# Performance work log

Measured on AMD Instinct MI355X. Metric: run time of the kernel, lower is better.

The kernel has to match this reference:

```python
import jax, jax.numpy as jnp
import numpy as np

N = 6000
E = 192000
H = 128
NUM_HEADS = 4

def _segsum(x, idx, n):
    return jax.ops.segment_sum(x, idx, num_segments=n)

def _gcn_encode(x, edges, W0, b0, Ws, bs):
    n = x.shape[0]
    sl = jnp.arange(n, dtype=edges.dtype)
    row = jnp.concatenate([edges[0], sl])  # source
    col = jnp.concatenate([edges[1], sl])  # target (aggregation)
    deg = _segsum(jnp.ones_like(col, dtype=x.dtype), col, n)
    dinv = jax.lax.rsqrt(deg)  # deg >= 1 thanks to self loops
    norm = (dinv[row] * dinv[col])[:, None]
    def layer(h, W, b):
        hw = h @ W
        agg = _segsum(hw[row] * norm, col, n)
        return jax.nn.relu(agg + b)
    h = layer(x, W0, b0)
    for i in range(Ws.shape[0]):
        h = layer(h, Ws[i], bs[i])
    return h

def setup_inputs() -> dict:
    key = jax.random.key(0)
    ks = jax.random.split(key, 24)
    def lin(k, fan_in, shape):
        return jax.random.normal(k, shape, dtype=jnp.float32) / np.sqrt(fan_in)
    return {
        'x_resting': jax.random.normal(ks[0], (N, 3), dtype=jnp.float32),
        'x_rigid': jax.random.normal(ks[1], (N, 3), dtype=jnp.float32),
        'edge_resting': jax.random.randint(ks[2], (2, E), 0, N, dtype=jnp.int32),
        'edge_rigid': jax.random.randint(ks[3], (2, E), 0, N, dtype=jnp.int32),
        'Wr0': lin(ks[4], 3, (3, H)), 'br0': jnp.zeros((H,), jnp.float32),
        'Wr': lin(ks[5], H, (2, H, H)), 'br': jnp.zeros((2, H), jnp.float32),
        'Wg0': lin(ks[6], 3, (3, H)), 'bg0': jnp.zeros((H,), jnp.float32),
        'Wg': lin(ks[7], H, (2, H, H)), 'bg': jnp.zeros((2, H), jnp.float32),
        'Wa': lin(ks[8], H, (NUM_HEADS, H, H)), 'ba': jnp.zeros((NUM_HEADS, H), jnp.float32),
        'Wd0': lin(ks[9], H * (NUM_HEADS + 1), (H * (NUM_HEADS + 1), H)), 'bd0': jnp.zeros((H,), jnp.float32),
        'Wd': lin(ks[10], H, (2, H, H)), 'bd': jnp.zeros((2, H), jnp.float32),
        'Wout': lin(ks[11], H, (H, 3)), 'bout': jnp.zeros((3,), jnp.float32),
    }

def reference(x_resting, x_rigid, edge_resting, edge_rigid,
              Wr0, br0, Wr, br, Wg0, bg0, Wg, bg,
              Wa, ba, Wd0, bd0, Wd, bd, Wout, bout):
    xr = _gcn_encode(x_resting, edge_resting, Wr0, br0, Wr, br)  # (N,H)
    xg = _gcn_encode(x_rigid, edge_rigid, Wg0, bg0, Wg, bg)      # (N,H)

    def head(W, b):
        q = xr @ W + b            # (N,H)
        k = xg @ W + b            # (N,H)
        attn = jax.nn.softmax(q @ k.T, axis=-1)  # (N,N) dense per head
        return attn @ xg          # (N,H)
    heads = jax.vmap(head)(Wa, ba)                       # (heads,N,H)
    pooled = heads.transpose(1, 0, 2).reshape(xr.shape[0], -1)  # (N, heads*H)

    h = jnp.concatenate([xr, pooled], axis=-1)  # (N, H*(heads+1))
    h = jax.nn.relu(h @ Wd0 + bd0)
    for i in range(Wd.shape[0]):
        h = jax.nn.relu(h @ Wd[i] + bd[i])
    return h @ Wout + bout  # (N, 3) deformed positions
```

## Files before the change

### kernel.cpp

```cpp
#include <hip/hip_runtime.h>
#include <math.h>

#define N_NODES 6000
#define N_EDGES 192000
#define H 128
#define NHEADS 4
#define HCAT 640
#define NPAD 6016
#define NTILES 188

typedef unsigned short ushort_t;
typedef __attribute__((ext_vector_type(8))) short short8;
typedef __attribute__((ext_vector_type(16))) float f32x16;

__device__ __forceinline__ void bf16split(float x, ushort_t& hi, ushort_t& lo) {
    unsigned ub = __float_as_uint(x);
    unsigned hb = ub & 0xffff0000u;
    float l = x - __uint_as_float(hb);
    hi = (ushort_t)(hb >> 16);
    lo = (ushort_t)(__float_as_uint(l) >> 16);
}

__device__ __forceinline__ void gll16(const ushort_t* g, ushort_t* l) {
    __builtin_amdgcn_global_load_lds((const __attribute__((address_space(1))) void*)g,
                                     (__attribute__((address_space(3))) void*)l, 16, 0, 0);
}

__global__ void zero_ints(int* p, int n) {
    int i = blockIdx.x * 256 + threadIdx.x;
    if (i < n) p[i] = 0;
}

__global__ void hist2(const int* __restrict__ eA, const int* __restrict__ eB,
                      int* __restrict__ cnt) {
    int e = blockIdx.x * 256 + threadIdx.x;
    int z = blockIdx.y;
    const int* edges = z ? eB : eA;
    if (e < N_EDGES) atomicAdd(&cnt[z * N_NODES + edges[N_EDGES + e]], 1);
}

__global__ __launch_bounds__(1024)
void scan2(const int* __restrict__ cnt_all, int* __restrict__ rs_all,
           float* __restrict__ dinv_all) {
    __shared__ int ps[1024];
    int z = blockIdx.x;
    const int* cnt = cnt_all + z * N_NODES;
    int* row_start = rs_all + z * (N_NODES + 1);
    float* dinv = dinv_all + z * N_NODES;
    int t = threadIdx.x;
    int base = t * 6;
    int local[6];
    int s = 0;
#pragma unroll
    for (int j = 0; j < 6; ++j) {
        int idx = base + j;
        int v = (idx < N_NODES) ? cnt[idx] : 0;
        local[j] = s;
        s += v;
        if (idx < N_NODES) dinv[idx] = rsqrtf((float)(v + 1));
    }
    ps[t] = s;
    __syncthreads();
    for (int off = 1; off < 1024; off <<= 1) {
        int v = (t >= off) ? ps[t - off] : 0;
        __syncthreads();
        ps[t] += v;
        __syncthreads();
    }
    int ex = (t > 0) ? ps[t - 1] : 0;
#pragma unroll
    for (int j = 0; j < 6; ++j) {
        int idx = base + j;
        if (idx < N_NODES) row_start[idx] = ex + local[j];
    }
    if (t == 1023) row_start[N_NODES] = ps[1023];
}

__global__ void place2(const int* __restrict__ eA, const int* __restrict__ eB,
                       const int* __restrict__ rs_all, int* __restrict__ cur_all,
                       int* __restrict__ eslot_all) {
    int e = blockIdx.x * 256 + threadIdx.x;
    int z = blockIdx.y;
    const int* edges = z ? eB : eA;
    if (e < N_EDGES) {
        int tg = edges[N_EDGES + e];
        int p = atomicAdd(&cur_all[z * N_NODES + tg], 1);
        eslot_all[(size_t)z * N_EDGES + rs_all[z * (N_NODES + 1) + tg] + p] = e;
    }
}

__global__ __launch_bounds__(256)
void gather_x3(const float* __restrict__ xA, const float* __restrict__ xB,
               const int* __restrict__ eA, const int* __restrict__ eB,
               const int* __restrict__ eslot_all, const int* __restrict__ rs_all,
               const float* __restrict__ dinv_all,
               float* __restrict__ outA, float* __restrict__ outB) {
    int z = blockIdx.y;
    int n = blockIdx.x * 256 + threadIdx.x;
    if (n >= N_NODES) return;
    const int* edges = z ? eB : eA;
    const int* eslot = eslot_all + (size_t)z * N_EDGES;
    const int* row_start = rs_all + z * (N_NODES + 1);
    const float* x = z ? xB : xA;
    const float* dv = dinv_all + z * N_NODES;
    float* out = z ? outB : outA;
    float di = dv[n];
    float a0 = x[n * 3 + 0] * di * di;
    float a1 = x[n * 3 + 1] * di * di;
    float a2 = x[n * 3 + 2] * di * di;
    int s0 = row_start[n], s1 = row_start[n + 1];
    for (int i = s0; i < s1; ++i) {
        int e = eslot[i];
        int s = edges[e];
        float nr = dv[s] * di;
        a0 += x[s * 3 + 0] * nr;
        a1 += x[s * 3 + 1] * nr;
        a2 += x[s * 3 + 2] * nr;
    }
    out[n * 3 + 0] = a0; out[n * 3 + 1] = a1; out[n * 3 + 2] = a2;
}

__global__ __launch_bounds__(256)
void gcn_gemm2(const float* __restrict__ hinA, const float* __restrict__ hinB,
               const float* __restrict__ WA, const float* __restrict__ WB,
               float* __restrict__ hwA, float* __restrict__ hwB, int in_dim,
               const float* __restrict__ bA, const float* __restrict__ bB, int do_relu) {
    __shared__ float xs[16 * H];
    int z = blockIdx.y;
    const float* hin = z ? hinB : hinA;
    const float* W = z ? WB : WA;
    float* hw = z ? hwB : hwA;
    const float* b = z ? bB : bA;
    int n0 = blockIdx.x * 16;
    int t = threadIdx.x;
    int f = t & (H - 1);
    int g = t >> 7;
    for (int i = t; i < 16 * H; i += 256) {
        int r = i >> 7, c = i & (H - 1);
        xs[i] = (c < in_dim) ? hin[(size_t)(n0 + r) * in_dim + c] : 0.f;
    }
    __syncthreads();
    float acc[8];
#pragma unroll
    for (int j = 0; j < 8; ++j) acc[j] = 0.f;
    for (int d = 0; d < in_dim; ++d) {
        float w = W[d * H + f];
#pragma unroll
        for (int j = 0; j < 8; ++j) acc[j] += xs[(g * 8 + j) * H + d] * w;
    }
    if (do_relu) {
        float bias = b[f];
#pragma unroll
        for (int j = 0; j < 8; ++j)
            hw[(size_t)(n0 + g * 8 + j) * H + f] = fmaxf(acc[j] + bias, 0.f);
    } else {
#pragma unroll
        for (int j = 0; j < 8; ++j) hw[(size_t)(n0 + g * 8 + j) * H + f] = acc[j];
    }
}

__global__ __launch_bounds__(H)
void gather2(const int* __restrict__ eA, const int* __restrict__ eB,
             const int* __restrict__ eslot_all, const int* __restrict__ rs_all,
             const float* __restrict__ hwA, const float* __restrict__ hwB,
             const float* __restrict__ dinv_all,
             const float* __restrict__ bA, const float* __restrict__ bB,
             float* __restrict__ outA, float* __restrict__ outB, int osA, int osB) {
    __shared__ int ssrc[128];
    __shared__ float snrm[128];
    int z = blockIdx.y;
    const int* edges = z ? eB : eA;
    const int* eslot = eslot_all + (size_t)z * N_EDGES;
    const int* row_start = rs_all + z * (N_NODES + 1);
    const float* hw = z ? hwB : hwA;
    const float* dinv = dinv_all + z * N_NODES;
    const float* b = z ? bB : bA;
    float* out = z ? outB : outA;
    int ostride = z ? osB : osA;

    int tg = blockIdx.x, f = threadIdx.x;
    int s0 = row_start[tg], s1 = row_start[tg + 1];
    float di = dinv[tg];
    float acc = hw[(size_t)tg * H + f] * di * di;
    for (int base = s0; base < s1; base += 128) {
        int cnt = min(128, s1 - base);
        __syncthreads();
        if (f < cnt) {
            int e = eslot[base + f];
            int s = edges[e];
            ssrc[f] = s;
            snrm[f] = dinv[s] * di;
        }
        __syncthreads();
        for (int i = 0; i < cnt; ++i)
            acc += hw[(size_t)ssrc[i] * H + f] * snrm[i];
    }
    float v = acc + b[f];
    out[(size_t)tg * ostride + f] = v > 0.f ? v : 0.f;
}

__global__ __launch_bounds__(256)
void qk_kernel2(const float* __restrict__ qs, int qstride, const float* __restrict__ xg,
                const float* __restrict__ Wa, const float* __restrict__ ba,
                ushort_t* __restrict__ Qh, ushort_t* __restrict__ Ql,
                ushort_t* __restrict__ Khs, ushort_t* __restrict__ Kls) {
    __shared__ float xs[2][16][H];
    int n0 = blockIdx.x * 16, head = blockIdx.y;
    int t = threadIdx.x;
    int f = t & (H - 1);
    int g = t >> 7;
    for (int i = t; i < 2 * 16 * H; i += 256) {
        int which = i >> 11;
        int rem = i & 2047;
        int row = rem >> 7, col = rem & 127;
        xs[which][row][col] = which ? xg[(size_t)(n0 + row) * H + col]
                                    : qs[(size_t)(n0 + row) * qstride + col];
    }
    __syncthreads();
    const float* W = Wa + (size_t)head * H * H;
    float bias = ba[head * H + f];
    float acc[16];
#pragma unroll
    for (int j = 0; j < 16; ++j) acc[j] = bias;
    for (int d = 0; d < H; ++d) {
        float w = W[d * H + f];
#pragma unroll
        for (int j = 0; j < 16; ++j) acc[j] += xs[g][j][d] * w;
    }
#pragma unroll
    for (int j = 0; j < 16; ++j) {
        int n = n0 + j;
        ushort_t hi, lo;
        bf16split(acc[j], hi, lo);
        if (g == 0) {
            size_t idx = ((size_t)(head * N_NODES + n) << 7) + f;
            Qh[idx] = hi; Ql[idx] = lo;
        } else {
            int pos = (((f >> 3) ^ (n & 15)) << 3) + (f & 7);
            size_t idx = ((size_t)(head * NPAD + n) << 7) + pos;
            Khs[idx] = hi; Kls[idx] = lo;
        }
    }
}

__global__ void zero_pad_k(ushort_t* __restrict__ Khs, ushort_t* __restrict__ Kls) {
    int i = blockIdx.x * 256 + threadIdx.x;
    if (i < NHEADS * 16 * H) {
        int head = i / (16 * H);
        int rest = i - head * 16 * H;
        int n = N_NODES + (rest >> 7);
        int f = rest & 127;
        size_t idx = ((size_t)(head * NPAD + n) << 7) + f;
        Khs[idx] = 0; Kls[idx] = 0;
    }
}

__global__ __launch_bounds__(128)
void cvt_vt(const float* __restrict__ xg, ushort_t* __restrict__ Vth, ushort_t* __restrict__ Vtl) {
    __shared__ float vs[32][129];
    int t0 = blockIdx.x;
    int t = threadIdx.x;
    for (int c = t; c < 32 * 32; c += 128) {
        int row = c >> 5, col4 = (c & 31) << 2;
        int n = t0 * 32 + row;
        float4 v = (n < N_NODES) ? *(const float4*)&xg[(size_t)n * H + col4]
                                 : float4{0.f, 0.f, 0.f, 0.f};
        vs[row][col4 + 0] = v.x; vs[row][col4 + 1] = v.y;
        vs[row][col4 + 2] = v.z; vs[row][col4 + 3] = v.w;
    }
    __syncthreads();
    int d = t;
    size_t base = ((size_t)t0 * H + d) * 32;
#pragma unroll
    for (int oc = 0; oc < 4; ++oc) {
        int cc = oc ^ (d & 3);
        unsigned uh[4], ul[4];
#pragma unroll
        for (int j = 0; j < 4; ++j) {
            ushort_t h0, l0, h1, l1;
            bf16split(vs[cc * 8 + 2 * j][d], h0, l0);
            bf16split(vs[cc * 8 + 2 * j + 1][d], h1, l1);
            uh[j] = (unsigned)h0 | ((unsigned)h1 << 16);
            ul[j] = (unsigned)l0 | ((unsigned)l1 << 16);
        }
        *(uint4*)&Vth[base + oc * 8] = make_uint4(uh[0], uh[1], uh[2], uh[3]);
        *(uint4*)&Vtl[base + oc * 8] = make_uint4(ul[0], ul[1], ul[2], ul[3]);
    }
}

__global__ __launch_bounds__(256, 2)
void attn_mfma7(const ushort_t* __restrict__ Qh, const ushort_t* __restrict__ Ql,
                const ushort_t* __restrict__ Khs, const ushort_t* __restrict__ Kls,
                const ushort_t* __restrict__ Vth, const ushort_t* __restrict__ Vtl,
                float* __restrict__ Opart, float* __restrict__ mlpart, int tps) {
    __shared__ ushort_t lds[2][4][4096];
    const int head = blockIdx.y;
    const int sp = blockIdx.z;
    const int t = threadIdx.x;
    const int lane = t & 63;
    const int w = t >> 6;
    const int r = lane & 31;
    const int h = lane >> 5;
    const int q0w = blockIdx.x * 128 + w * 32;

    int t_begin = sp * tps;
    int t_end = t_begin + tps; if (t_end > NTILES) t_end = NTILES;

    const size_t kbase = (size_t)head * NPAD * H;
    const int o1 = t * 8, o2 = t * 8 + 2048;

    int qr = q0w + r; if (qr > N_NODES - 1) qr = N_NODES - 1;
    const size_t qbase = ((size_t)(head * N_NODES + qr)) << 7;
    short8 qfh[8], qfl[8];
#pragma unroll
    for (int s = 0; s < 8; ++s) {
        qfh[s] = *(const short8*)&Qh[qbase + 16 * s + 8 * h];
        qfl[s] = *(const short8*)&Ql[qbase + 16 * s + 8 * h];
    }

    f32x16 O[4];
#pragma unroll
    for (int sub = 0; sub < 4; ++sub)
#pragma unroll
        for (int i = 0; i < 16; ++i) O[sub][i] = 0.f;
    float mrun = -1e30f, lrun = 0.f;
    short8 aPh[2], aPl[2];
    float alpha_prev = 1.f;
    int resc_prev = 0;

    {
        const ushort_t* sKh = Khs + kbase + (size_t)t_begin * 4096;
        const ushort_t* sKl = Kls + kbase + (size_t)t_begin * 4096;
        gll16(sKh + o1, &lds[0][0][o1]); gll16(sKh + o2, &lds[0][0][o2]);
        gll16(sKl + o1, &lds[0][1][o1]); gll16(sKl + o2, &lds[0][1][o2]);
    }

    for (int it = t_begin; it < t_end; ++it) {
        const int b = (it - t_begin) & 1;
        __syncthreads();
        {
            int nt = it + 1; if (nt >= t_end) nt = t_begin;
            const ushort_t* sKh = Khs + kbase + (size_t)nt * 4096;
            const ushort_t* sKl = Kls + kbase + (size_t)nt * 4096;
            const ushort_t* sVh = Vth + (size_t)it * 4096;
            const ushort_t* sVl = Vtl + (size_t)it * 4096;
            gll16(sKh + o1, &lds[b ^ 1][0][o1]); gll16(sKh + o2, &lds[b ^ 1][0][o2]);
            gll16(sKl + o1, &lds[b ^ 1][1][o1]); gll16(sKl + o2, &lds[b ^ 1][1][o2]);
            gll16(sVh + o1, &lds[b ^ 1][2][o1]); gll16(sVh + o2, &lds[b ^ 1][2][o2]);
            gll16(sVl + o1, &lds[b ^ 1][3][o1]); gll16(sVl + o2, &lds[b ^ 1][3][o2]);
        }
        const ushort_t* lKh = &lds[b][0][0];
        const ushort_t* lKl = &lds[b][1][0];
        const ushort_t* lVh = &lds[b][2][0];
        const ushort_t* lVl = &lds[b][3][0];

        f32x16 acc;
#pragma unroll
        for (int i = 0; i < 16; ++i) acc[i] = 0.f;
        const int krow = r * H;
#pragma unroll
        for (int s = 0; s < 8; ++s) {
            int cc = ((2 * s + h) ^ (r & 15)) << 3;
            short8 ah = *(const short8*)&lKh[krow + cc];
            short8 al = *(const short8*)&lKl[krow + cc];
            acc = __builtin_amdgcn_mfma_f32_32x32x16_bf16(ah, qfh[s], acc, 0, 0, 0);
            acc = __builtin_amdgcn_mfma_f32_32x32x16_bf16(ah, qfl[s], acc, 0, 0, 0);
            acc = __builtin_amdgcn_mfma_f32_32x32x16_bf16(al, qfh[s], acc, 0, 0, 0);
        }

        if (it != t_begin) {
            if (resc_prev) {
#pragma unroll
                for (int i = 0; i < 16; ++i) {
                    int rowq = (i & 3) + 8 * (i >> 2) + 4 * h;
                    float a = __shfl(alpha_prev, rowq);
#pragma unroll
                    for (int sub = 0; sub < 4; ++sub) O[sub][i] *= a;
                }
            }
#pragma unroll
            for (int sub = 0; sub < 4; ++sub) {
                const int vrow = (32 * sub + r) * 32;
#pragma unroll
                for (int s2 = 0; s2 < 2; ++s2) {
                    int cc = (((2 * s2 + h) ^ (r & 3)) << 3);
                    short8 bh = *(const short8*)&lVh[vrow + cc];
                    short8 bl = *(const short8*)&lVl[vrow + cc];
                    O[sub] = __builtin_amdgcn_mfma_f32_32x32x16_bf16(aPh[s2], bh, O[sub], 0, 0, 0);
                    O[sub] = __builtin_amdgcn_mfma_f32_32x32x16_bf16(aPh[s2], bl, O[sub], 0, 0, 0);
                    O[sub] = __builtin_amdgcn_mfma_f32_32x32x16_bf16(aPl[s2], bh, O[sub], 0, 0, 0);
                }
            }
        }

        float sv[16];
#pragma unroll
        for (int i = 0; i < 16; ++i) sv[i] = acc[i];
        int klim = N_NODES - (it << 5);
        if (klim < 32) {
#pragma unroll
            for (int i = 0; i < 16; ++i) {
                int row = (i & 3) + 8 * (i >> 2) + 4 * h;
                if (row >= klim) sv[i] = -1e30f;
            }
        }
        float tmax = sv[0];
#pragma unroll
        for (int i = 1; i < 16; ++i) tmax = fmaxf(tmax, sv[i]);
        tmax = fmaxf(tmax, __shfl_xor(tmax, 32));
        float mnew = fmaxf(mrun, tmax);
        float p[16];
        float psum = 0.f;
#pragma unroll
        for (int i = 0; i < 16; ++i) { p[i] = __expf(sv[i] - mnew); psum += p[i]; }

        if (__ballot(mnew > mrun)) {
            float alpha = __expf(mrun - mnew);
            lrun *= alpha;
            alpha_prev = alpha;
            resc_prev = 1;
        } else {
            resc_prev = 0;
        }
        lrun += psum;
        mrun = mnew;

        float pr[16];
#pragma unroll
        for (int i = 0; i < 16; ++i) pr[i] = __shfl_xor(p[i], 32);
#pragma unroll
        for (int s2 = 0; s2 < 2; ++s2) {
#pragma unroll
            for (int j = 0; j < 8; ++j) {
                int c = j & 3;
                float v;
                if (j < 4) v = (h == 0) ? p[c + 8 * s2] : pr[c + 8 * s2 + 4];
                else       v = (h == 1) ? p[c + 8 * s2 + 4] : pr[c + 8 * s2];
                unsigned ub = __float_as_uint(v);
                unsigned hb = ub & 0xffff0000u;
                float lo = v - __uint_as_float(hb);
                aPh[s2][j] = (short)(hb >> 16);
                aPl[s2][j] = (short)(__float_as_uint(lo) >> 16);
            }
        }
    }

    __syncthreads();
    {
        const int bl = (t_end - t_begin) & 1;
        const ushort_t* lVh = &lds[bl][2][0];
        const ushort_t* lVl = &lds[bl][3][0];
        if (resc_prev) {
#pragma unroll
            for (int i = 0; i < 16; ++i) {
                int rowq = (i & 3) + 8 * (i >> 2) + 4 * h;
                float a = __shfl(alpha_prev, rowq);
#pragma unroll
                for (int sub = 0; sub < 4; ++sub) O[sub][i] *= a;
            }
        }
#pragma unroll
        for (int sub = 0; sub < 4; ++sub) {
            const int vrow = (32 * sub + r) * 32;
#pragma unroll
            for (int s2 = 0; s2 < 2; ++s2) {
                int cc = (((2 * s2 + h) ^ (r & 3)) << 3);
                short8 bh = *(const short8*)&lVh[vrow + cc];
                short8 bl = *(const short8*)&lVl[vrow + cc];
                O[sub] = __builtin_amdgcn_mfma_f32_32x32x16_bf16(aPh[s2], bh, O[sub], 0, 0, 0);
                O[sub] = __builtin_amdgcn_mfma_f32_32x32x16_bf16(aPh[s2], bl, O[sub], 0, 0, 0);
                O[sub] = __builtin_amdgcn_mfma_f32_32x32x16_bf16(aPl[s2], bh, O[sub], 0, 0, 0);
            }
        }
    }

    lrun += __shfl_xor(lrun, 32);

    float* Ob = Opart + (size_t)(sp * NHEADS + head) * NPAD * H;
#pragma unroll
    for (int i = 0; i < 16; ++i) {
        int rowq = (i & 3) + 8 * (i >> 2) + 4 * h;
        int qg = q0w + rowq;
        if (qg < N_NODES) {
            float* dst = &Ob[(size_t)qg * H + r];
#pragma unroll
            for (int sub = 0; sub < 4; ++sub) dst[32 * sub] = O[sub][i];
        }
    }
    if (h == 0 && q0w + r < N_NODES) {
        float2* ml = (float2*)mlpart;
        ml[(size_t)(sp * NHEADS + head) * NPAD + q0w + r] = make_float2(mrun, lrun);
    }
}

__global__ __launch_bounds__(256)
void attn_combine(const float* __restrict__ Opart, const float* __restrict__ mlpart,
                  float* __restrict__ hcat, int ns) {
    int idx = blockIdx.x * 256 + threadIdx.x;
    if (idx >= NHEADS * N_NODES * (H / 4)) return;
    int head = idx / (N_NODES * (H / 4));
    int rest = idx - head * N_NODES * (H / 4);
    int q = rest >> 5;
    int d4 = (rest & 31) << 2;
    const float2* ml = (const float2*)mlpart;
    float m = -1e30f;
    for (int s = 0; s < ns; ++s)
        m = fmaxf(m, ml[(size_t)(s * NHEADS + head) * NPAD + q].x);
    float lsum = 0.f;
    float4 o = {0.f, 0.f, 0.f, 0.f};
    for (int s = 0; s < ns; ++s) {
        float2 v = ml[(size_t)(s * NHEADS + head) * NPAD + q];
        float wgt = __expf(v.x - m);
        lsum += v.y * wgt;
        float4 ov = *(const float4*)&Opart[((size_t)(s * NHEADS + head) * NPAD + q) * H + d4];
        o.x += ov.x * wgt; o.y += ov.y * wgt; o.z += ov.z * wgt; o.w += ov.w * wgt;
    }
    float inv = 1.f / lsum;
    float4 res = {o.x * inv, o.y * inv, o.z * inv, o.w * inv};
    *(float4*)&hcat[(size_t)q * HCAT + H + head * H + d4] = res;
}

__global__ __launch_bounds__(256)
void decoder(const float* __restrict__ hcat,
             const float* __restrict__ Wd0, const float* __restrict__ bd0,
             const float* __restrict__ Wd, const float* __restrict__ bd,
             const float* __restrict__ Wout, const float* __restrict__ bout,
             float* __restrict__ out) {
    __shared__ float s0[8 * HCAT];
    __shared__ float s1[8 * H];
    __shared__ float s2[8 * H];
    int n0 = blockIdx.x * 8;
    int t = threadIdx.x;
    int f = t & (H - 1);
    int g = t >> 7;
    for (int i = t; i < 8 * HCAT; i += 256)
        s0[i] = hcat[(size_t)n0 * HCAT + i];
    __syncthreads();

    float acc[4];
#pragma unroll
    for (int j = 0; j < 4; ++j) acc[j] = bd0[f];
    for (int d = 0; d < HCAT; ++d) {
        float w = Wd0[d * H + f];
#pragma unroll
        for (int j = 0; j < 4; ++j) acc[j] += s0[(g * 4 + j) * HCAT + d] * w;
    }
#pragma unroll
    for (int j = 0; j < 4; ++j) s1[(g * 4 + j) * H + f] = fmaxf(acc[j], 0.f);
    __syncthreads();

#pragma unroll
    for (int j = 0; j < 4; ++j) acc[j] = bd[f];
    for (int d = 0; d < H; ++d) {
        float w = Wd[d * H + f];
#pragma unroll
        for (int j = 0; j < 4; ++j) acc[j] += s1[(g * 4 + j) * H + d] * w;
    }
#pragma unroll
    for (int j = 0; j < 4; ++j) s2[(g * 4 + j) * H + f] = fmaxf(acc[j], 0.f);
    __syncthreads();

#pragma unroll
    for (int j = 0; j < 4; ++j) acc[j] = bd[H + f];
    for (int d = 0; d < H; ++d) {
        float w = Wd[H * H + d * H + f];
#pragma unroll
        for (int j = 0; j < 4; ++j) acc[j] += s2[(g * 4 + j) * H + d] * w;
    }
    __syncthreads();
#pragma unroll
    for (int j = 0; j < 4; ++j) s1[(g * 4 + j) * H + f] = fmaxf(acc[j], 0.f);
    __syncthreads();

    if (t < 24) {
        int n = t / 3, c = t % 3;
        float o = bout[c];
        for (int d = 0; d < H; ++d) o += s1[n * H + d] * Wout[d * 3 + c];
        out[(size_t)(n0 + n) * 3 + c] = o;
    }
}

extern "C" void kernel_launch(void* const* d_in, const int* in_sizes, int n_in,
                              void* d_out, int out_size, void* d_ws, size_t ws_size,
                              hipStream_t stream) {
    const float* x_rest = (const float*)d_in[0];
    const float* x_rig  = (const float*)d_in[1];
    const int*   e_rest = (const int*)d_in[2];
    const int*   e_rig  = (const int*)d_in[3];
    const float* Wr0 = (const float*)d_in[4];
    const float* br0 = (const float*)d_in[5];
    const float* Wr  = (const float*)d_in[6];
    const float* br  = (const float*)d_in[7];
    const float* Wg0 = (const float*)d_in[8];
    const float* bg0 = (const float*)d_in[9];
    const float* Wg  = (const float*)d_in[10];
    const float* bg  = (const float*)d_in[11];
    const float* Wa  = (const float*)d_in[12];
    const float* ba  = (const float*)d_in[13];
    const float* Wd0 = (const float*)d_in[14];
    const float* bd0 = (const float*)d_in[15];
    const float* Wd  = (const float*)d_in[16];
    const float* bd  = (const float*)d_in[17];
    const float* Wout = (const float*)d_in[18];
    const float* bout = (const float*)d_in[19];
    float* out = (float*)d_out;

    const size_t NH = (size_t)N_NODES * H;
    float* ws = (float*)d_ws;
    float* dinv = ws;
    float* hw   = dinv + 2 * N_NODES;
    float* hb   = hw + 2 * NH;
    float* hcat = hb + 2 * NH;
    float* ha   = hcat;
    float* xg   = hb + NH;
    float* xagg = hb;
    ushort_t* Qh  = (ushort_t*)(hcat + (size_t)N_NODES * HCAT);
    ushort_t* Ql  = Qh + (size_t)NHEADS * N_NODES * H;
    ushort_t* Khs = Ql + (size_t)NHEADS * N_NODES * H;
    ushort_t* Kls = Khs + (size_t)NHEADS * NPAD * H;
    ushort_t* Vth = Kls + (size_t)NHEADS * NPAD * H;
    ushort_t* Vtl = Vth + (size_t)NTILES * H * 32;
    int* ib   = (int*)(Vtl + (size_t)NTILES * H * 32);
    int* cnt  = ib;
    int* cur  = cnt + 2 * N_NODES;
    int* rs   = cur + 2 * N_NODES;
    int* eslot = rs + 2 * (N_NODES + 1);
    int* iend  = eslot + 2 * N_EDGES;
    float* Opart = (float*)(((uintptr_t)iend + 15) & ~(uintptr_t)15);

    size_t base_bytes = (size_t)((char*)Opart - (char*)d_ws);
    size_t per_split  = (size_t)NHEADS * NPAD * (H + 2) * sizeof(float);
    int NS = 2;
    if (ws_size >= base_bytes + 5 * per_split + (1u << 20)) NS = 5;
    else if (ws_size >= base_bytes + 4 * per_split + (1u << 20)) NS = 4;
    float* mlpart = Opart + (size_t)NS * NHEADS * NPAD * H;
    int tps = (NTILES + NS - 1) / NS;

    const int gN = (N_NODES + 255) / 256;
    const int gE = (N_EDGES + 255) / 256;

    zero_ints<<<(4 * N_NODES + 255) / 256, 256, 0, stream>>>(cnt, 4 * N_NODES);
    hist2<<<dim3(gE, 2), 256, 0, stream>>>(e_rest, e_rig, cnt);
    scan2<<<2, 1024, 0, stream>>>(cnt, rs, dinv);
    place2<<<dim3(gE, 2), 256, 0, stream>>>(e_rest, e_rig, rs, cur, eslot);

    float* hw_r = hw, * hw_g = hw + NH;
    float* ha_r = ha, * ha_g = ha + NH;
    float* hb_r = hb, * hb_g = hb + NH;
    float* xagg_r = xagg, * xagg_g = xagg + 3 * N_NODES;

    gather_x3<<<dim3(gN, 2), 256, 0, stream>>>(x_rest, x_rig, e_rest, e_rig, eslot, rs,
                                               dinv, xagg_r, xagg_g);
    gcn_gemm2<<<dim3(N_NODES / 16, 2), 256, 0, stream>>>(xagg_r, xagg_g, Wr0, Wg0,
                                                         ha_r, ha_g, 3, br0, bg0, 1);
    gcn_gemm2<<<dim3(N_NODES / 16, 2), 256, 0, stream>>>(ha_r, ha_g, Wr, Wg, hw_r, hw_g, H,
                                                         nullptr, nullptr, 0);
    gather2<<<dim3(N_NODES, 2), H, 0, stream>>>(e_rest, e_rig, eslot, rs, hw_r, hw_g, dinv,
                                                br, bg, hb_r, hb_g, H, H);
    gcn_gemm2<<<dim3(N_NODES / 16, 2), 256, 0, stream>>>(hb_r, hb_g, Wr + H * H, Wg + H * H,
                                                         hw_r, hw_g, H, nullptr, nullptr, 0);
    gather2<<<dim3(N_NODES, 2), H, 0, stream>>>(e_rest, e_rig, eslot, rs, hw_r, hw_g, dinv,
                                                br + H, bg + H, hcat, xg, HCAT, H);

    qk_kernel2<<<dim3(N_NODES / 16, NHEADS), 256, 0, stream>>>(hcat, HCAT, xg, Wa, ba,
                                                               Qh, Ql, Khs, Kls);
    zero_pad_k<<<(NHEADS * 16 * H + 255) / 256, 256, 0, stream>>>(Khs, Kls);
    cvt_vt<<<NTILES, 128, 0, stream>>>(xg, Vth, Vtl);
    attn_mfma7<<<dim3(47, NHEADS, NS), 256, 0, stream>>>(Qh, Ql, Khs, Kls, Vth, Vtl,
                                                         Opart, mlpart, tps);
    attn_combine<<<(NHEADS * N_NODES * (H / 4) + 255) / 256, 256, 0, stream>>>(Opart, mlpart,
                                                                               hcat, NS);

    decoder<<<N_NODES / 8, 256, 0, stream>>>(hcat, Wd0, bd0, Wd, bd, Wout, bout, out);
}
```

Before: 610.9 us.

## Fold log2e into Q, fuse attention combine into decoder, stagger block starts

```diff
diff --git a/kernel.cpp b/kernel.cpp
--- a/kernel.cpp
+++ b/kernel.cpp
@@ -8,6 +8,7 @@
 #define HCAT 640
 #define NPAD 6016
 #define NTILES 188
+#define LOG2E 1.4426950408889634f
 
 typedef unsigned short ushort_t;
 typedef __attribute__((ext_vector_type(8))) short short8;
@@ -165,7 +166,7 @@
              const float* __restrict__ hwA, const float* __restrict__ hwB,
              const float* __restrict__ dinv_all,
              const float* __restrict__ bA, const float* __restrict__ bB,
-             float* __restrict__ outA, float* __restrict__ outB, int osA, int osB) {
+             float* __restrict__ outA, float* __restrict__ outB) {
     __shared__ int ssrc[128];
     __shared__ float snrm[128];
     int z = blockIdx.y;
@@ -176,7 +177,6 @@
     const float* dinv = dinv_all + z * N_NODES;
     const float* b = z ? bB : bA;
     float* out = z ? outB : outA;
-    int ostride = z ? osB : osA;
 
     int tg = blockIdx.x, f = threadIdx.x;
     int s0 = row_start[tg], s1 = row_start[tg + 1];
@@ -196,11 +196,11 @@
             acc += hw[(size_t)ssrc[i] * H + f] * snrm[i];
     }
     float v = acc + b[f];
-    out[(size_t)tg * ostride + f] = v > 0.f ? v : 0.f;
+    out[(size_t)tg * H + f] = v > 0.f ? v : 0.f;
 }
 
 __global__ __launch_bounds__(256)
-void qk_kernel2(const float* __restrict__ qs, int qstride, const float* __restrict__ xg,
+void qk_kernel2(const float* __restrict__ qs, const float* __restrict__ xg,
                 const float* __restrict__ Wa, const float* __restrict__ ba,
                 ushort_t* __restrict__ Qh, ushort_t* __restrict__ Ql,
                 ushort_t* __restrict__ Khs, ushort_t* __restrict__ Kls) {
@@ -214,7 +214,7 @@
         int rem = i & 2047;
         int row = rem >> 7, col = rem & 127;
         xs[which][row][col] = which ? xg[(size_t)(n0 + row) * H + col]
-                                    : qs[(size_t)(n0 + row) * qstride + col];
+                                    : qs[(size_t)(n0 + row) * H + col];
     }
     __syncthreads();
     const float* W = Wa + (size_t)head * H * H;
@@ -231,11 +231,12 @@
     for (int j = 0; j < 16; ++j) {
         int n = n0 + j;
         ushort_t hi, lo;
-        bf16split(acc[j], hi, lo);
         if (g == 0) {
+            bf16split(acc[j] * LOG2E, hi, lo);
             size_t idx = ((size_t)(head * N_NODES + n) << 7) + f;
             Qh[idx] = hi; Ql[idx] = lo;
         } else {
+            bf16split(acc[j], hi, lo);
             int pos = (((f >> 3) ^ (n & 15)) << 3) + (f & 7);
             size_t idx = ((size_t)(head * NPAD + n) << 7) + pos;
             Khs[idx] = hi; Kls[idx] = lo;
@@ -289,7 +290,7 @@
 }
 
 __global__ __launch_bounds__(256, 2)
-void attn_mfma7(const ushort_t* __restrict__ Qh, const ushort_t* __restrict__ Ql,
+void attn_mfma8(const ushort_t* __restrict__ Qh, const ushort_t* __restrict__ Ql,
                 const ushort_t* __restrict__ Khs, const ushort_t* __restrict__ Kls,
                 const ushort_t* __restrict__ Vth, const ushort_t* __restrict__ Vtl,
                 float* __restrict__ Opart, float* __restrict__ mlpart, int tps) {
@@ -298,9 +299,9 @@
     const int sp = blockIdx.z;
     const int t = threadIdx.x;
     const int lane = t & 63;
-    const int w = t >> 6;
     const int r = lane & 31;
     const int h = lane >> 5;
+    const int w = t >> 6;
     const int q0w = blockIdx.x * 128 + w * 32;
 
     int t_begin = sp * tps;
@@ -333,6 +334,12 @@
         const ushort_t* sKl = Kls + kbase + (size_t)t_begin * 4096;
         gll16(sKh + o1, &lds[0][0][o1]); gll16(sKh + o2, &lds[0][0][o2]);
         gll16(sKl + o1, &lds[0][1][o1]); gll16(sKl + o2, &lds[0][1][o2]);
+    }
+
+    {
+        unsigned lin = blockIdx.x + 47u * (blockIdx.y + (unsigned)NHEADS * blockIdx.z);
+        unsigned ph = (lin * 2654435761u) >> 29;
+        for (unsigned i = 0; i < ph; ++i) __builtin_amdgcn_s_sleep(12);
     }
 
     for (int it = t_begin; it < t_end; ++it) {
@@ -412,10 +419,10 @@
         float p[16];
         float psum = 0.f;
 #pragma unroll
-        for (int i = 0; i < 16; ++i) { p[i] = __expf(sv[i] - mnew); psum += p[i]; }
+        for (int i = 0; i < 16; ++i) { p[i] = exp2f(sv[i] - mnew); psum += p[i]; }
 
         if (__ballot(mnew > mrun)) {
-            float alpha = __expf(mrun - mnew);
+            float alpha = exp2f(mrun - mnew);
             lrun *= alpha;
             alpha_prev = alpha;
             resc_prev = 1;
@@ -494,34 +501,8 @@
 }
 
 __global__ __launch_bounds__(256)
-void attn_combine(const float* __restrict__ Opart, const float* __restrict__ mlpart,
-                  float* __restrict__ hcat, int ns) {
-    int idx = blockIdx.x * 256 + threadIdx.x;
-    if (idx >= NHEADS * N_NODES * (H / 4)) return;
-    int head = idx / (N_NODES * (H / 4));
-    int rest = idx - head * N_NODES * (H / 4);
-    int q = rest >> 5;
-    int d4 = (rest & 31) << 2;
-    const float2* ml = (const float2*)mlpart;
-    float m = -1e30f;
-    for (int s = 0; s < ns; ++s)
-        m = fmaxf(m, ml[(size_t)(s * NHEADS + head) * NPAD + q].x);
-    float lsum = 0.f;
-    float4 o = {0.f, 0.f, 0.f, 0.f};
-    for (int s = 0; s < ns; ++s) {
-        float2 v = ml[(size_t)(s * NHEADS + head) * NPAD + q];
-        float wgt = __expf(v.x - m);
-        lsum += v.y * wgt;
-        float4 ov = *(const float4*)&Opart[((size_t)(s * NHEADS + head) * NPAD + q) * H + d4];
-        o.x += ov.x * wgt; o.y += ov.y * wgt; o.z += ov.z * wgt; o.w += ov.w * wgt;
-    }
-    float inv = 1.f / lsum;
-    float4 res = {o.x * inv, o.y * inv, o.z * inv, o.w * inv};
-    *(float4*)&hcat[(size_t)q * HCAT + H + head * H + d4] = res;
-}
-
-__global__ __launch_bounds__(256)
-void decoder(const float* __restrict__ hcat,
+void decoder(const float* __restrict__ xr,
+             const float* __restrict__ Opart, const float* __restrict__ mlpart, int ns,
              const float* __restrict__ Wd0, const float* __restrict__ bd0,
              const float* __restrict__ Wd, const float* __restrict__ bd,
              const float* __restrict__ Wout, const float* __restrict__ bout,
@@ -533,8 +514,30 @@
     int t = threadIdx.x;
     int f = t & (H - 1);
     int g = t >> 7;
-    for (int i = t; i < 8 * HCAT; i += 256)
-        s0[i] = hcat[(size_t)n0 * HCAT + i];
+    const float2* ml = (const float2*)mlpart;
+
+    for (int i = t; i < 8 * H; i += 256) {
+        int n = i >> 7;
+        s0[n * HCAT + (i & 127)] = xr[(size_t)(n0 + n) * H + (i & 127)];
+    }
+    for (int i = t; i < 8 * 512; i += 256) {
+        int n = i >> 9;
+        int rem = i & 511;
+        int head = rem >> 7;
+        int d = rem & 127;
+        int q = n0 + n;
+        float m = -1e30f;
+        for (int s = 0; s < ns; ++s)
+            m = fmaxf(m, ml[(size_t)(s * NHEADS + head) * NPAD + q].x);
+        float lsum = 0.f, o = 0.f;
+        for (int s = 0; s < ns; ++s) {
+            float2 v = ml[(size_t)(s * NHEADS + head) * NPAD + q];
+            float wgt = exp2f(v.x - m);
+            lsum += v.y * wgt;
+            o += Opart[((size_t)(s * NHEADS + head) * NPAD + q) * H + d] * wgt;
+        }
+        s0[n * HCAT + H + head * H + d] = o / lsum;
+    }
     __syncthreads();
 
     float acc[4];
@@ -610,11 +613,11 @@
     float* dinv = ws;
     float* hw   = dinv + 2 * N_NODES;
     float* hb   = hw + 2 * NH;
-    float* hcat = hb + 2 * NH;
-    float* ha   = hcat;
+    float* xr   = hb + 2 * NH;
+    float* hx   = xr + NH;
     float* xg   = hb + NH;
     float* xagg = hb;
-    ushort_t* Qh  = (ushort_t*)(hcat + (size_t)N_NODES * HCAT);
+    ushort_t* Qh  = (ushort_t*)(hx + NH);
     ushort_t* Ql  = Qh + (size_t)NHEADS * N_NODES * H;
     ushort_t* Khs = Ql + (size_t)NHEADS * N_NODES * H;
     ushort_t* Kls = Khs + (size_t)NHEADS * NPAD * H;
@@ -645,7 +648,7 @@
     place2<<<dim3(gE, 2), 256, 0, stream>>>(e_rest, e_rig, rs, cur, eslot);
 
     float* hw_r = hw, * hw_g = hw + NH;
-    float* ha_r = ha, * ha_g = ha + NH;
+    float* ha_r = xr, * ha_g = hx;
     float* hb_r = hb, * hb_g = hb + NH;
     float* xagg_r = xagg, * xagg_g = xagg + 3 * N_NODES;
 
@@ -656,20 +659,19 @@
     gcn_gemm2<<<dim3(N_NODES / 16, 2), 256, 0, stream>>>(ha_r, ha_g, Wr, Wg, hw_r, hw_g, H,
                                                          nullptr, nullptr, 0);
     gather2<<<dim3(N_NODES, 2), H, 0, stream>>>(e_rest, e_rig, eslot, rs, hw_r, hw_g, dinv,
-                                                br, bg, hb_r, hb_g, H, H);
+                                                br, bg, hb_r, hb_g);
     gcn_gemm2<<<dim3(N_NODES / 16, 2), 256, 0, stream>>>(hb_r, hb_g, Wr + H * H, Wg + H * H,
                                                          hw_r, hw_g, H, nullptr, nullptr, 0);
     gather2<<<dim3(N_NODES, 2), H, 0, stream>>>(e_rest, e_rig, eslot, rs, hw_r, hw_g, dinv,
-                                                br + H, bg + H, hcat, xg, HCAT, H);
-
-    qk_kernel2<<<dim3(N_NODES / 16, NHEADS), 256, 0, stream>>>(hcat, HCAT, xg, Wa, ba,
+                                                br + H, bg + H, xr, xg);
+
+    qk_kernel2<<<dim3(N_NODES / 16, NHEADS), 256, 0, stream>>>(xr, xg, Wa, ba,
                                                                Qh, Ql, Khs, Kls);
     zero_pad_k<<<(NHEADS * 16 * H + 255) / 256, 256, 0, stream>>>(Khs, Kls);
     cvt_vt<<<NTILES, 128, 0, stream>>>(xg, Vth, Vtl);
-    attn_mfma7<<<dim3(47, NHEADS, NS), 256, 0, stream>>>(Qh, Ql, Khs, Kls, Vth, Vtl,
+    attn_mfma8<<<dim3(47, NHEADS, NS), 256, 0, stream>>>(Qh, Ql, Khs, Kls, Vth, Vtl,
                                                          Opart, mlpart, tps);
-    attn_combine<<<(NHEADS * N_NODES * (H / 4) + 255) / 256, 256, 0, stream>>>(Opart, mlpart,
-                                                                               hcat, NS);
-
-    decoder<<<N_NODES / 8, 256, 0, stream>>>(hcat, Wd0, bd0, Wd, bd, Wout, bout, out);
-}
+
+    decoder<<<N_NODES / 8, 256, 0, stream>>>(xr, Opart, mlpart, NS,
+                                             Wd0, bd0, Wd, bd, Wout, bout, out);
+}
```

New measurement: 665.0 us. 8.9% more time.
